# Optimization experiments

Hardware: AMD Instinct MI355X
Metric: run time of the kernel (lower is better)

The kernel has to match this reference:

```python
import jax, jax.numpy as jnp
import numpy as np

N = 100000      # nodes
E = 1600000     # edges (avg degree 16)
D = 128         # feature dim (in_dim == out_dim)
ALPHA = 0.1     # initial-residual mixing
BETA = 0.5      # identity-mapping / linear mixing


def setup_inputs() -> dict:
    key = jax.random.key(0)
    k1, k2, k3, k4, k5 = jax.random.split(key, 5)
    features = jax.random.normal(k1, (N, D), dtype=jnp.float32)
    initial_features = jax.random.normal(k2, (N, D), dtype=jnp.float32)
    # xavier_uniform with relu gain sqrt(2): bound = gain * sqrt(6/(fan_in+fan_out))
    bound = np.sqrt(2.0) * np.sqrt(6.0 / (D + D))
    W = jax.random.uniform(k5, (D, D), dtype=jnp.float32, minval=-bound, maxval=bound)
    src = jax.random.randint(k3, (E,), 0, N, dtype=jnp.int32)
    dst = jax.random.randint(k4, (E,), 0, N, dtype=jnp.int32)
    return {"features": features, "initial_features": initial_features,
            "W": W, "src": src, "dst": dst}


def reference(features, initial_features, W, src, dst):
    # symmetric degree normalization (edge weights are all ones)
    degs = jax.ops.segment_sum(jnp.ones((E,), features.dtype), dst, num_segments=N)
    norm = jnp.power(jnp.maximum(degs, 1.0), -0.5)[:, None]          # [N,1]
    h = features * norm                                               # [N,D]
    # message passing: m_e = h[src_e] * w_e (w=1); aggregate sum into dst
    agg = jax.ops.segment_sum(h[src], dst, num_segments=N)            # [N,D]
    h = agg * norm
    # alpha initial-residual, beta identity-mapped linear combine
    h = (1.0 - ALPHA) * h + ALPHA * initial_features
    h = (1.0 - BETA) * h + BETA * (h @ W.T)
    return jax.nn.relu(h)
```

## Files before the change

### kernel.cpp

```cpp
#include <hip/hip_runtime.h>
#include <math.h>

#define D 128
#define THREADS 256
#define BS 512
#define MAXB 1024
#define BIN_T 512
#define EPT 16
#define BIN_CHUNK (BIN_T * EPT)

typedef __attribute__((ext_vector_type(8))) short s16x8;
typedef __attribute__((ext_vector_type(4))) float f32x4;
typedef __attribute__((ext_vector_type(4))) float f4;
typedef __attribute__((ext_vector_type(4))) unsigned u4;

__device__ __forceinline__ unsigned short f2bf(float f) {
    unsigned u = __float_as_uint(f);
    u += 0x7FFFu + ((u >> 16) & 1u);
    return (unsigned short)(u >> 16);
}
__device__ __forceinline__ float bflo(unsigned u) { return __uint_as_float(u << 16); }
__device__ __forceinline__ float bfhi(unsigned u) { return __uint_as_float(u & 0xFFFF0000u); }


__global__ __launch_bounds__(THREADS) void k_hist(const int* __restrict__ dst,
                                                  int* __restrict__ bcnt,
                                                  int E, int nbuck) {
    __shared__ int lh[MAXB];
    for (int b = threadIdx.x; b < nbuck; b += THREADS) lh[b] = 0;
    __syncthreads();
    const int stride = gridDim.x * THREADS;
    for (int e = blockIdx.x * THREADS + threadIdx.x; e < E; e += stride)
        atomicAdd(&lh[dst[e] >> 9], 1);
    __syncthreads();
    for (int b = threadIdx.x; b < nbuck; b += THREADS) {
        const int v = lh[b];
        if (v) atomicAdd(&bcnt[b], v);
    }
}

__global__ __launch_bounds__(MAXB) void k_scan(const int* __restrict__ bcnt,
                                               int* __restrict__ bbase,
                                               int* __restrict__ bcur, int nbuck) {
    __shared__ int sh[MAXB];
    const int tid = threadIdx.x;
    const int v = (tid < nbuck) ? bcnt[tid] : 0;
    sh[tid] = v;
    __syncthreads();
    for (int s = 1; s < MAXB; s <<= 1) {
        const int t = (tid >= s) ? sh[tid - s] : 0;
        __syncthreads();
        sh[tid] += t;
        __syncthreads();
    }
    if (tid < nbuck) {
        const int ex = sh[tid] - v;
        bbase[tid] = ex;
        bcur[tid] = ex;
    }
    if (tid == nbuck - 1) bbase[nbuck] = sh[tid];
}

__global__ __launch_bounds__(BIN_T) void k_bin(const int* __restrict__ src,
                                               const int* __restrict__ dst,
                                               int* __restrict__ bcur,
                                               unsigned* __restrict__ ebuf,
                                               int E, int nbuck) {
    __shared__ int lh[MAXB];
    __shared__ int lbase[MAXB];
    const int tid = threadIdx.x;
    for (int b = tid; b < nbuck; b += BIN_T) lh[b] = 0;
    __syncthreads();
    const int base = blockIdx.x * BIN_CHUNK;
    int bk[EPT];
    unsigned pk[EPT];
#pragma unroll
    for (int k = 0; k < EPT; ++k) {
        const int e = base + k * BIN_T + tid;
        if (e < E) {
            const int d = dst[e];
            bk[k] = d >> 9;
            pk[k] = ((unsigned)src[e] << 9) | (unsigned)(d & (BS - 1));
            atomicAdd(&lh[bk[k]], 1);
        } else {
            bk[k] = -1;
        }
    }
    __syncthreads();
    for (int b = tid; b < nbuck; b += BIN_T) {
        const int v = lh[b];
        lbase[b] = v ? atomicAdd(&bcur[b], v) : 0;
        lh[b] = 0;
    }
    __syncthreads();
#pragma unroll
    for (int k = 0; k < EPT; ++k) {
        if (bk[k] >= 0) {
            const int pos = lbase[bk[k]] + atomicAdd(&lh[bk[k]], 1);
            ebuf[pos] = pk[k];
        }
    }
}

__global__ __launch_bounds__(BS) void k_csr(const int* __restrict__ bbase,
                                            const unsigned* __restrict__ ebuf,
                                            int* __restrict__ csr,
                                            int* __restrict__ off,
                                            float* __restrict__ normf,
                                            int n, int nbuck) {
    __shared__ int cnt[BS];
    __shared__ int ex[BS];
    const int b = blockIdx.x, tid = threadIdx.x;
    const int lo = bbase[b], hi = bbase[b + 1];
    cnt[tid] = 0;
    __syncthreads();
    for (int e = lo + tid; e < hi; e += BS)
        atomicAdd(&cnt[ebuf[e] & (BS - 1)], 1);
    __syncthreads();
    const int deg = cnt[tid];
    ex[tid] = deg;
    __syncthreads();
    for (int s = 1; s < BS; s <<= 1) {
        const int t = (tid >= s) ? ex[tid - s] : 0;
        __syncthreads();
        ex[tid] += t;
        __syncthreads();
    }
    const int excl = ex[tid] - deg;
    const int node = b * BS + tid;
    if (node < n) {
        off[node] = lo + excl;
        normf[node] = rsqrtf(fmaxf((float)deg, 1.0f));
    }
    if (b == nbuck - 1 && tid == 0) off[n] = bbase[nbuck];
    cnt[tid] = excl;
    __syncthreads();
    for (int e = lo + tid; e < hi; e += BS) {
        const unsigned pe = ebuf[e];
        const int p = atomicAdd(&cnt[pe & (BS - 1)], 1);
        csr[lo + p] = (int)(pe >> 9);
    }
}

__global__ __launch_bounds__(THREADS) void k_scale(
    const float* __restrict__ f, const float* __restrict__ nrm,
    uint4* __restrict__ hb, int n) {
    int c = blockIdx.x * THREADS + threadIdx.x;
    if (c >= n * 16) return;
    float nv = nrm[c >> 4];
    const f4* fp = (const f4*)f;
    const f4 a = __builtin_nontemporal_load(fp + c * 2);
    const f4 b = __builtin_nontemporal_load(fp + c * 2 + 1);
    uint4 o;
    o.x = f2bf(a.x * nv) | ((unsigned)f2bf(a.y * nv) << 16);
    o.y = f2bf(a.z * nv) | ((unsigned)f2bf(a.w * nv) << 16);
    o.z = f2bf(b.x * nv) | ((unsigned)f2bf(b.y * nv) << 16);
    o.w = f2bf(b.z * nv) | ((unsigned)f2bf(b.w * nv) << 16);
    hb[c] = o;
}

__global__ __launch_bounds__(THREADS) void k_gather_csr(
    const uint4* __restrict__ hb, const float* __restrict__ initf,
    const int* __restrict__ off, const int* __restrict__ csr,
    const float* __restrict__ normf, uint4* __restrict__ tb, int n) {
    const int g = (blockIdx.x * THREADS + threadIdx.x) >> 4;
    if (g >= n) return;
    const int gl = threadIdx.x & 15;

    float acc[8] = {0.f, 0.f, 0.f, 0.f, 0.f, 0.f, 0.f, 0.f};

#define ROW(S)                                                      \
    {                                                               \
        const uint4 r = hb[(size_t)(S)*16 + gl];                    \
        acc[0] += bflo(r.x); acc[1] += bfhi(r.x);                   \
        acc[2] += bflo(r.y); acc[3] += bfhi(r.y);                   \
        acc[4] += bflo(r.z); acc[5] += bfhi(r.z);                   \
        acc[6] += bflo(r.w); acc[7] += bfhi(r.w);                   \
    }
    const int begin = off[g], end = off[g + 1];
    int j = begin;
    for (; j + 4 <= end; j += 4) {
        const int s0 = csr[j], s1 = csr[j + 1], s2 = csr[j + 2], s3 = csr[j + 3];
        ROW(s0); ROW(s1); ROW(s2); ROW(s3);
    }
    for (; j < end; ++j) ROW(csr[j]);
#undef ROW

    const float nv = 0.9f * normf[g];
    const f4* iv = (const f4*)(initf + (size_t)g * D);
    const f4 i0 = __builtin_nontemporal_load(iv + gl * 2);
    const f4 i1 = __builtin_nontemporal_load(iv + gl * 2 + 1);
    float t[8];
    t[0] = nv * acc[0] + 0.1f * i0.x; t[1] = nv * acc[1] + 0.1f * i0.y;
    t[2] = nv * acc[2] + 0.1f * i0.z; t[3] = nv * acc[3] + 0.1f * i0.w;
    t[4] = nv * acc[4] + 0.1f * i1.x; t[5] = nv * acc[5] + 0.1f * i1.y;
    t[6] = nv * acc[6] + 0.1f * i1.z; t[7] = nv * acc[7] + 0.1f * i1.w;
    u4 o;
    o.x = f2bf(t[0]) | ((unsigned)f2bf(t[1]) << 16);
    o.y = f2bf(t[2]) | ((unsigned)f2bf(t[3]) << 16);
    o.z = f2bf(t[4]) | ((unsigned)f2bf(t[5]) << 16);
    o.w = f2bf(t[6]) | ((unsigned)f2bf(t[7]) << 16);
    __builtin_nontemporal_store(o, (u4*)tb + (size_t)g * 16 + gl);
}

__device__ __forceinline__ void stage_M(const float* __restrict__ W,
                                        uint4* __restrict__ sMt, int tid) {
    for (int c = tid; c < D * 16; c += THREADS) {
        const int j = c >> 4, kc = c & 15;
        const float* wr = W + j * D + kc * 8;
        float m[8];
#pragma unroll
        for (int q = 0; q < 8; ++q) m[q] = 0.5f * wr[q];
        const int dj = j - kc * 8;
        if (dj >= 0 && dj < 8) m[dj] += 0.5f;
        uint4 o;
        o.x = f2bf(m[0]) | ((unsigned)f2bf(m[1]) << 16);
        o.y = f2bf(m[2]) | ((unsigned)f2bf(m[3]) << 16);
        o.z = f2bf(m[4]) | ((unsigned)f2bf(m[5]) << 16);
        o.w = f2bf(m[6]) | ((unsigned)f2bf(m[7]) << 16);
        sMt[j * 16 + (kc ^ (j & 7))] = o;
    }
}

__device__ __forceinline__ void gemm_tile(const uint4* __restrict__ sMt,
                                          const uint4* __restrict__ sT,
                                          float* __restrict__ out,
                                          int base, int n, int lane, int wave) {
    const int l15 = lane & 15, lq = lane >> 4;
    const int mt = wave & 1, ntb = (wave >> 1) * 4;
    const int nr = mt * 16 + l15;
    s16x8 a[4];
#pragma unroll
    for (int ks = 0; ks < 4; ++ks)
        a[ks] = *reinterpret_cast<const s16x8*>(
            &sT[nr * 16 + ((ks * 4 + lq) ^ (nr & 7))]);

#pragma unroll
    for (int tnt = 0; tnt < 4; ++tnt) {
        const int nt = ntb + tnt;
        const int jr = nt * 16 + l15;
        f32x4 c = {0.f, 0.f, 0.f, 0.f};
#pragma unroll
        for (int ks = 0; ks < 4; ++ks) {
            const s16x8 b = *reinterpret_cast<const s16x8*>(
                &sMt[jr * 16 + ((ks * 4 + lq) ^ (jr & 7))]);
            c = __builtin_amdgcn_mfma_f32_16x16x32_bf16(a[ks], b, c, 0, 0, 0);
        }
        const int col = nt * 16 + l15;
        const int row0 = base + mt * 16 + lq * 4;
#pragma unroll
        for (int r = 0; r < 4; ++r) {
            const int node = row0 + r;
            if (node < n)
                __builtin_nontemporal_store(fmaxf(c[r], 0.f),
                                            &out[(size_t)node * D + col]);
        }
    }
}

__global__ __launch_bounds__(THREADS) void k_gemm_tb(
    const float* __restrict__ W, const uint4* __restrict__ tb,
    float* __restrict__ out, int n, int numTiles) {
    __shared__ uint4 sMt[D * 16];
    __shared__ uint4 sT[32 * 16];
    const int tid = threadIdx.x;
    stage_M(W, sMt, tid);
    __syncthreads();

    const int sn = tid >> 3;
    const int c0 = (tid & 7) * 2;
    const int wave = tid >> 6, lane = tid & 63;

    for (int tile = blockIdx.x; tile < numTiles; tile += gridDim.x) {
        const int base = tile << 5;
        {
            const int node = base + sn;
#pragma unroll
            for (int s = 0; s < 2; ++s) {
                const int cc = c0 + s;
                uint4 o;
                if (node < n) {
                    const u4 t = __builtin_nontemporal_load(
                        (const u4*)tb + (size_t)node * 16 + cc);
                    o.x = t.x; o.y = t.y; o.z = t.z; o.w = t.w;
                } else {
                    o.x = o.y = o.z = o.w = 0u;
                }
                sT[sn * 16 + (cc ^ (sn & 7))] = o;
            }
        }
        __syncthreads();
        gemm_tile(sMt, sT, out, base, n, lane, wave);
        __syncthreads();
    }
}

__global__ __launch_bounds__(THREADS) void k_build1(
    const int* __restrict__ src, const int* __restrict__ dst,
    int* __restrict__ head, int2* __restrict__ p, int E) {
    int e = blockIdx.x * THREADS + threadIdx.x;
    if (e < E) {
        int nx = atomicExch(&head[dst[e]], e);
        p[e] = make_int2(nx, src[e]);
    }
}

__global__ __launch_bounds__(THREADS) void k_normwalk1(
    const int* __restrict__ head, const int2* __restrict__ p,
    float* __restrict__ normf, int n) {
    int i = blockIdx.x * THREADS + threadIdx.x;
    if (i >= n) return;
    int c = head[i], cnt = 0;
    while (c >= 0) { ++cnt; c = p[c].x; }
    normf[i] = rsqrtf(fmaxf((float)cnt, 1.0f));
}

__global__ __launch_bounds__(THREADS) void k_gatherchain(
    const float* __restrict__ features, const float* __restrict__ initf,
    const int* __restrict__ head, const int2* __restrict__ p,
    const float* __restrict__ normf, float* __restrict__ out, int n) {
    const int g = (blockIdx.x * THREADS + threadIdx.x) >> 4;
    if (g >= n) return;
    const int gl = threadIdx.x & 15;
    float acc[8] = {0.f, 0.f, 0.f, 0.f, 0.f, 0.f, 0.f, 0.f};
    int c = head[g];
    while (c >= 0) {
        const int2 pc = p[c];
        const float w = normf[pc.y];
        const float4* fr = (const float4*)(features + (size_t)pc.y * D);
        const float4 f0 = fr[gl * 2], f1 = fr[gl * 2 + 1];
        acc[0] += f0.x * w; acc[1] += f0.y * w;
        acc[2] += f0.z * w; acc[3] += f0.w * w;
        acc[4] += f1.x * w; acc[5] += f1.y * w;
        acc[6] += f1.z * w; acc[7] += f1.w * w;
        c = pc.x;
    }
    const float nv = 0.9f * normf[g];
    const float4* iv = (const float4*)(initf + (size_t)g * D);
    const float4 i0 = iv[gl * 2], i1 = iv[gl * 2 + 1];
    float4 t0, t1;
    t0.x = nv * acc[0] + 0.1f * i0.x; t0.y = nv * acc[1] + 0.1f * i0.y;
    t0.z = nv * acc[2] + 0.1f * i0.z; t0.w = nv * acc[3] + 0.1f * i0.w;
    t1.x = nv * acc[4] + 0.1f * i1.x; t1.y = nv * acc[5] + 0.1f * i1.y;
    t1.z = nv * acc[6] + 0.1f * i1.z; t1.w = nv * acc[7] + 0.1f * i1.w;
    float4* orow = (float4*)(out + (size_t)g * D);
    orow[gl * 2] = t0;
    orow[gl * 2 + 1] = t1;
}

__global__ __launch_bounds__(THREADS) void k_gemm_ip(
    const float* __restrict__ W, float* __restrict__ out, int n, int numTiles) {
    __shared__ uint4 sMt[D * 16];
    __shared__ uint4 sT[32 * 16];
    const int tid = threadIdx.x;
    stage_M(W, sMt, tid);
    __syncthreads();
    const int sn = tid >> 3;
    const int c0 = (tid & 7) * 2;
    const int wave = tid >> 6, lane = tid & 63;
    for (int tile = blockIdx.x; tile < numTiles; tile += gridDim.x) {
        const int base = tile << 5;
        {
            const int node = base + sn;
#pragma unroll
            for (int s = 0; s < 2; ++s) {
                const int cc = c0 + s;
                uint4 o;
                if (node < n) {
                    const float4* tr = (const float4*)(out + (size_t)node * D);
                    const float4 a = tr[cc * 2], b = tr[cc * 2 + 1];
                    o.x = f2bf(a.x) | ((unsigned)f2bf(a.y) << 16);
                    o.y = f2bf(a.z) | ((unsigned)f2bf(a.w) << 16);
                    o.z = f2bf(b.x) | ((unsigned)f2bf(b.y) << 16);
                    o.w = f2bf(b.z) | ((unsigned)f2bf(b.w) << 16);
                } else {
                    o.x = o.y = o.z = o.w = 0u;
                }
                sT[sn * 16 + (cc ^ (sn & 7))] = o;
            }
        }
        __syncthreads();
        gemm_tile(sMt, sT, out, base, n, lane, wave);
        __syncthreads();
    }
}

extern "C" void kernel_launch(void* const* d_in, const int* in_sizes, int n_in,
                              void* d_out, int out_size, void* d_ws, size_t ws_size,
                              hipStream_t stream) {
    const float* features = (const float*)d_in[0];
    const float* initf    = (const float*)d_in[1];
    const float* W        = (const float*)d_in[2];
    const int*   src      = (const int*)d_in[3];
    const int*   dst      = (const int*)d_in[4];
    float* out = (float*)d_out;

    const int n = in_sizes[0] / D;
    const int E = in_sizes[3];
    if (n <= 0) return;

    const int nbuck = (n + BS - 1) / BS;
    const int numTiles = (n + 31) >> 5;
    const int gridT = numTiles < 1024 ? numTiles : 1024;
    const int gridG = (int)(((size_t)n * 16 + THREADS - 1) / THREADS);

    const size_t nA   = ((size_t)n * 4 + 15) & ~(size_t)15;
    const size_t oA   = ((size_t)(n + 1) * 4 + 15) & ~(size_t)15;
    const size_t bA   = ((size_t)(MAXB + 1) * 4 + 15) & ~(size_t)15;
    const size_t eA   = ((size_t)E * 4 + 15) & ~(size_t)15;
    const size_t cA   = ((size_t)E * 4 + 15) & ~(size_t)15;
    const size_t hbA  = (size_t)n * 256;
    const size_t tbA  = (size_t)n * 256;
    const size_t needMain = nA + oA + 3 * bA + eA + cA + hbA + tbA;

    if (nbuck <= MAXB && n <= (1 << 23) && ws_size >= needMain) {
        char* w = (char*)d_ws;
        float*    normf = (float*)w;              w += nA;
        int*      off   = (int*)w;                w += oA;
        int*      bcnt  = (int*)w;                w += bA;
        int*      bbase = (int*)w;                w += bA;
        int*      bcur  = (int*)w;                w += bA;
        unsigned* ebuf  = (unsigned*)w;           w += eA;
        int*      csr   = (int*)w;                w += cA;
        uint4*    hb    = (uint4*)w;              w += hbA;
        uint4*    tb    = (uint4*)w;

        hipMemsetAsync(bcnt, 0, (size_t)(MAXB + 1) * 4, stream);
        k_hist<<<256, THREADS, 0, stream>>>(dst, bcnt, E, nbuck);
        k_scan<<<1, MAXB, 0, stream>>>(bcnt, bbase, bcur, nbuck);
        k_bin<<<(E + BIN_CHUNK - 1) / BIN_CHUNK, BIN_T, 0, stream>>>(
            src, dst, bcur, ebuf, E, nbuck);
        k_csr<<<nbuck, BS, 0, stream>>>(bbase, ebuf, csr, off, normf, n, nbuck);
        k_scale<<<(n * 16 + THREADS - 1) / THREADS, THREADS, 0, stream>>>(
            features, normf, hb, n);
        k_gather_csr<<<gridG, THREADS, 0, stream>>>(hb, initf, off, csr, normf, tb, n);
        k_gemm_tb<<<gridT, THREADS, 0, stream>>>(W, tb, out, n, numTiles);
    } else {
        const size_t pA = ((size_t)E * 8 + 15) & ~(size_t)15;
        float* normf = (float*)d_ws;
        int*   head  = (int*)((char*)d_ws + nA);
        int2*  p     = (int2*)((char*)d_ws + 2 * nA);
        if (ws_size < 2 * nA + pA) return;
        hipMemsetAsync(head, 0xFF, (size_t)n * 4, stream);
        k_build1<<<(E + THREADS - 1) / THREADS, THREADS, 0, stream>>>(src, dst, head, p, E);
        k_normwalk1<<<(n + THREADS - 1) / THREADS, THREADS, 0, stream>>>(head, p, normf, n);
        k_gatherchain<<<gridG, THREADS, 0, stream>>>(features, initf, head, p, normf, out, n);
        k_gemm_ip<<<gridT, THREADS, 0, stream>>>(W, out, n, numTiles);
    }
}
```

Before: 186.2 us.

## Fuse feature scaling into CSR build, partition edges by source quarter, widen gather

The CSR build now sorts each node's neighbor list into four source-index ranges and stores the per-range counts, so the gather visits source rows in phases that roughly match the source-row partition and should improve L2 locality of the bf16 feature reads. The separate scale kernel is folded into the CSR kernel, which removes one launch. The gather now gives each node 64 threads (four sub-groups striding over its edges) and combines them with cross-lane shuffles, trading fewer nodes per block for more memory parallelism per node. The histogram kernel also reads dst as int4 vectors. The costs are a larger shared-memory count array in the CSR kernel and per-range counts capped at 16 bits.

Measured after the change: 194.6 us. +4.5%, slower.

```diff
diff --git a/kernel.cpp b/kernel.cpp
--- a/kernel.cpp
+++ b/kernel.cpp
@@ -22,7 +22,6 @@
 __device__ __forceinline__ float bflo(unsigned u) { return __uint_as_float(u << 16); }
 __device__ __forceinline__ float bfhi(unsigned u) { return __uint_as_float(u & 0xFFFF0000u); }
 
-
 __global__ __launch_bounds__(THREADS) void k_hist(const int* __restrict__ dst,
                                                   int* __restrict__ bcnt,
                                                   int E, int nbuck) {
@@ -30,8 +29,17 @@
     for (int b = threadIdx.x; b < nbuck; b += THREADS) lh[b] = 0;
     __syncthreads();
     const int stride = gridDim.x * THREADS;
-    for (int e = blockIdx.x * THREADS + threadIdx.x; e < E; e += stride)
-        atomicAdd(&lh[dst[e] >> 9], 1);
+    const int E4 = E >> 2;
+    const int4* dst4 = (const int4*)dst;
+    for (int i = blockIdx.x * THREADS + threadIdx.x; i < E4; i += stride) {
+        const int4 d = dst4[i];
+        atomicAdd(&lh[d.x >> 9], 1);
+        atomicAdd(&lh[d.y >> 9], 1);
+        atomicAdd(&lh[d.z >> 9], 1);
+        atomicAdd(&lh[d.w >> 9], 1);
+    }
+    if (blockIdx.x == 0 && threadIdx.x < (E & 3))
+        atomicAdd(&lh[dst[(E & ~3) + threadIdx.x] >> 9], 1);
     __syncthreads();
     for (int b = threadIdx.x; b < nbuck; b += THREADS) {
         const int v = lh[b];
@@ -104,20 +112,30 @@
 
 __global__ __launch_bounds__(BS) void k_csr(const int* __restrict__ bbase,
                                             const unsigned* __restrict__ ebuf,
+                                            const float* __restrict__ features,
                                             int* __restrict__ csr,
                                             int* __restrict__ off,
+                                            uint2* __restrict__ pcnt,
                                             float* __restrict__ normf,
-                                            int n, int nbuck) {
-    __shared__ int cnt[BS];
+                                            uint4* __restrict__ hb,
+                                            int n, int nbuck, unsigned cut) {
+    __shared__ int cnt[BS * 4];
     __shared__ int ex[BS];
     const int b = blockIdx.x, tid = threadIdx.x;
     const int lo = bbase[b], hi = bbase[b + 1];
-    cnt[tid] = 0;
-    __syncthreads();
-    for (int e = lo + tid; e < hi; e += BS)
-        atomicAdd(&cnt[ebuf[e] & (BS - 1)], 1);
-    __syncthreads();
-    const int deg = cnt[tid];
+#pragma unroll
+    for (int q = 0; q < 4; ++q) cnt[tid * 4 + q] = 0;
+    __syncthreads();
+    for (int e = lo + tid; e < hi; e += BS) {
+        const unsigned pe = ebuf[e];
+        const unsigned s = pe >> 9;
+        const int q = (s >= cut) + (s >= 2 * cut) + (s >= 3 * cut);
+        atomicAdd(&cnt[(int)(pe & (BS - 1)) * 4 + q], 1);
+    }
+    __syncthreads();
+    int c0 = cnt[tid * 4], c1 = cnt[tid * 4 + 1],
+        c2 = cnt[tid * 4 + 2], c3 = cnt[tid * 4 + 3];
+    const int deg = c0 + c1 + c2 + c3;
     ex[tid] = deg;
     __syncthreads();
     for (int s = 1; s < BS; s <<= 1) {
@@ -128,79 +146,97 @@
     }
     const int excl = ex[tid] - deg;
     const int node = b * BS + tid;
+    const float nrm = rsqrtf(fmaxf((float)deg, 1.0f));
     if (node < n) {
         off[node] = lo + excl;
-        normf[node] = rsqrtf(fmaxf((float)deg, 1.0f));
+        pcnt[node] = make_uint2((unsigned)c0 | ((unsigned)c1 << 16),
+                                (unsigned)c2 | ((unsigned)c3 << 16));
+        normf[node] = nrm;
     }
     if (b == nbuck - 1 && tid == 0) off[n] = bbase[nbuck];
-    cnt[tid] = excl;
-    __syncthreads();
+    int run = excl;
+    cnt[tid * 4 + 0] = run; run += c0;
+    cnt[tid * 4 + 1] = run; run += c1;
+    cnt[tid * 4 + 2] = run; run += c2;
+    cnt[tid * 4 + 3] = run;
+    __syncthreads();
+    ex[tid] = __float_as_int(nrm);
     for (int e = lo + tid; e < hi; e += BS) {
         const unsigned pe = ebuf[e];
-        const int p = atomicAdd(&cnt[pe & (BS - 1)], 1);
-        csr[lo + p] = (int)(pe >> 9);
-    }
-}
-
-__global__ __launch_bounds__(THREADS) void k_scale(
-    const float* __restrict__ f, const float* __restrict__ nrm,
-    uint4* __restrict__ hb, int n) {
-    int c = blockIdx.x * THREADS + threadIdx.x;
-    if (c >= n * 16) return;
-    float nv = nrm[c >> 4];
-    const f4* fp = (const f4*)f;
-    const f4 a = __builtin_nontemporal_load(fp + c * 2);
-    const f4 b = __builtin_nontemporal_load(fp + c * 2 + 1);
-    uint4 o;
-    o.x = f2bf(a.x * nv) | ((unsigned)f2bf(a.y * nv) << 16);
-    o.y = f2bf(a.z * nv) | ((unsigned)f2bf(a.w * nv) << 16);
-    o.z = f2bf(b.x * nv) | ((unsigned)f2bf(b.y * nv) << 16);
-    o.w = f2bf(b.z * nv) | ((unsigned)f2bf(b.w * nv) << 16);
-    hb[c] = o;
+        const unsigned s = pe >> 9;
+        const int q = (s >= cut) + (s >= 2 * cut) + (s >= 3 * cut);
+        const int p = atomicAdd(&cnt[(int)(pe & (BS - 1)) * 4 + q], 1);
+        csr[lo + p] = (int)s;
+    }
+    __syncthreads();
+    const f4* fp = (const f4*)features;
+    for (int idx = tid; idx < BS * 16; idx += BS) {
+        const int nl = idx >> 4;
+        const int gnode = b * BS + nl;
+        if (gnode >= n) break;
+        const float nv = __int_as_float(ex[nl]);
+        const size_t C = (size_t)gnode * 16 + (idx & 15);
+        const f4 a = __builtin_nontemporal_load(fp + C * 2);
+        const f4 bb = __builtin_nontemporal_load(fp + C * 2 + 1);
+        uint4 o;
+        o.x = f2bf(a.x * nv) | ((unsigned)f2bf(a.y * nv) << 16);
+        o.y = f2bf(a.z * nv) | ((unsigned)f2bf(a.w * nv) << 16);
+        o.z = f2bf(bb.x * nv) | ((unsigned)f2bf(bb.y * nv) << 16);
+        o.w = f2bf(bb.z * nv) | ((unsigned)f2bf(bb.w * nv) << 16);
+        hb[C] = o;
+    }
 }
 
 __global__ __launch_bounds__(THREADS) void k_gather_csr(
     const uint4* __restrict__ hb, const float* __restrict__ initf,
-    const int* __restrict__ off, const int* __restrict__ csr,
-    const float* __restrict__ normf, uint4* __restrict__ tb, int n) {
-    const int g = (blockIdx.x * THREADS + threadIdx.x) >> 4;
+    const int* __restrict__ off, const uint2* __restrict__ pcnt,
+    const int* __restrict__ csr, const float* __restrict__ normf,
+    uint4* __restrict__ tb, int n) {
+    const int g = blockIdx.x * 4 + (threadIdx.x >> 6);
     if (g >= n) return;
+    const int sub = (threadIdx.x >> 4) & 3;
     const int gl = threadIdx.x & 15;
 
     float acc[8] = {0.f, 0.f, 0.f, 0.f, 0.f, 0.f, 0.f, 0.f};
-
-#define ROW(S)                                                      \
-    {                                                               \
-        const uint4 r = hb[(size_t)(S)*16 + gl];                    \
-        acc[0] += bflo(r.x); acc[1] += bfhi(r.x);                   \
-        acc[2] += bflo(r.y); acc[3] += bfhi(r.y);                   \
-        acc[4] += bflo(r.z); acc[5] += bfhi(r.z);                   \
-        acc[6] += bflo(r.w); acc[7] += bfhi(r.w);                   \
-    }
-    const int begin = off[g], end = off[g + 1];
-    int j = begin;
-    for (; j + 4 <= end; j += 4) {
-        const int s0 = csr[j], s1 = csr[j + 1], s2 = csr[j + 2], s3 = csr[j + 3];
-        ROW(s0); ROW(s1); ROW(s2); ROW(s3);
-    }
-    for (; j < end; ++j) ROW(csr[j]);
-#undef ROW
-
-    const float nv = 0.9f * normf[g];
-    const f4* iv = (const f4*)(initf + (size_t)g * D);
-    const f4 i0 = __builtin_nontemporal_load(iv + gl * 2);
-    const f4 i1 = __builtin_nontemporal_load(iv + gl * 2 + 1);
-    float t[8];
-    t[0] = nv * acc[0] + 0.1f * i0.x; t[1] = nv * acc[1] + 0.1f * i0.y;
-    t[2] = nv * acc[2] + 0.1f * i0.z; t[3] = nv * acc[3] + 0.1f * i0.w;
-    t[4] = nv * acc[4] + 0.1f * i1.x; t[5] = nv * acc[5] + 0.1f * i1.y;
-    t[6] = nv * acc[6] + 0.1f * i1.z; t[7] = nv * acc[7] + 0.1f * i1.w;
-    u4 o;
-    o.x = f2bf(t[0]) | ((unsigned)f2bf(t[1]) << 16);
-    o.y = f2bf(t[2]) | ((unsigned)f2bf(t[3]) << 16);
-    o.z = f2bf(t[4]) | ((unsigned)f2bf(t[5]) << 16);
-    o.w = f2bf(t[6]) | ((unsigned)f2bf(t[7]) << 16);
-    __builtin_nontemporal_store(o, (u4*)tb + (size_t)g * 16 + gl);
+    int j = off[g];
+    const uint2 pc = pcnt[g];
+    const int lens[4] = {(int)(pc.x & 0xFFFFu), (int)(pc.x >> 16),
+                         (int)(pc.y & 0xFFFFu), (int)(pc.y >> 16)};
+#pragma unroll 1
+    for (int p = 0; p < 4; ++p) {
+        const int end = j + lens[p];
+        for (int jj = j + sub; jj < end; jj += 4) {
+            const int s = csr[jj];
+            const uint4 r = hb[(size_t)s * 16 + gl];
+            acc[0] += bflo(r.x); acc[1] += bfhi(r.x);
+            acc[2] += bflo(r.y); acc[3] += bfhi(r.y);
+            acc[4] += bflo(r.z); acc[5] += bfhi(r.z);
+            acc[6] += bflo(r.w); acc[7] += bfhi(r.w);
+        }
+        j = end;
+    }
+#pragma unroll
+    for (int q = 0; q < 8; ++q) {
+        acc[q] += __shfl_xor(acc[q], 16);
+        acc[q] += __shfl_xor(acc[q], 32);
+    }
+    if (sub == 0) {
+        const float nv = 0.9f * normf[g];
+        const f4* iv = (const f4*)(initf + (size_t)g * D);
+        const f4 i0 = __builtin_nontemporal_load(iv + gl * 2);
+        const f4 i1 = __builtin_nontemporal_load(iv + gl * 2 + 1);
+        float t[8];
+        t[0] = nv * acc[0] + 0.1f * i0.x; t[1] = nv * acc[1] + 0.1f * i0.y;
+        t[2] = nv * acc[2] + 0.1f * i0.z; t[3] = nv * acc[3] + 0.1f * i0.w;
+        t[4] = nv * acc[4] + 0.1f * i1.x; t[5] = nv * acc[5] + 0.1f * i1.y;
+        t[6] = nv * acc[6] + 0.1f * i1.z; t[7] = nv * acc[7] + 0.1f * i1.w;
+        u4 o;
+        o.x = f2bf(t[0]) | ((unsigned)f2bf(t[1]) << 16);
+        o.y = f2bf(t[2]) | ((unsigned)f2bf(t[3]) << 16);
+        o.z = f2bf(t[4]) | ((unsigned)f2bf(t[5]) << 16);
+        o.w = f2bf(t[6]) | ((unsigned)f2bf(t[7]) << 16);
+        __builtin_nontemporal_store(o, (u4*)tb + (size_t)g * 16 + gl);
+    }
 }
 
 __device__ __forceinline__ void stage_M(const float* __restrict__ W,
@@ -402,21 +438,22 @@
     const int nbuck = (n + BS - 1) / BS;
     const int numTiles = (n + 31) >> 5;
     const int gridT = numTiles < 1024 ? numTiles : 1024;
-    const int gridG = (int)(((size_t)n * 16 + THREADS - 1) / THREADS);
 
     const size_t nA   = ((size_t)n * 4 + 15) & ~(size_t)15;
     const size_t oA   = ((size_t)(n + 1) * 4 + 15) & ~(size_t)15;
+    const size_t pcA  = ((size_t)n * 8 + 15) & ~(size_t)15;
     const size_t bA   = ((size_t)(MAXB + 1) * 4 + 15) & ~(size_t)15;
     const size_t eA   = ((size_t)E * 4 + 15) & ~(size_t)15;
     const size_t cA   = ((size_t)E * 4 + 15) & ~(size_t)15;
     const size_t hbA  = (size_t)n * 256;
     const size_t tbA  = (size_t)n * 256;
-    const size_t needMain = nA + oA + 3 * bA + eA + cA + hbA + tbA;
+    const size_t needMain = nA + oA + pcA + 3 * bA + eA + cA + hbA + tbA;
 
     if (nbuck <= MAXB && n <= (1 << 23) && ws_size >= needMain) {
         char* w = (char*)d_ws;
         float*    normf = (float*)w;              w += nA;
         int*      off   = (int*)w;                w += oA;
+        uint2*    pcnt  = (uint2*)w;              w += pcA;
         int*      bcnt  = (int*)w;                w += bA;
         int*      bbase = (int*)w;                w += bA;
         int*      bcur  = (int*)w;                w += bA;
@@ -425,15 +462,17 @@
         uint4*    hb    = (uint4*)w;              w += hbA;
         uint4*    tb    = (uint4*)w;
 
+        const unsigned cut = ((unsigned)n + 3) >> 2;
+
         hipMemsetAsync(bcnt, 0, (size_t)(MAXB + 1) * 4, stream);
         k_hist<<<256, THREADS, 0, stream>>>(dst, bcnt, E, nbuck);
         k_scan<<<1, MAXB, 0, stream>>>(bcnt, bbase, bcur, nbuck);
         k_bin<<<(E + BIN_CHUNK - 1) / BIN_CHUNK, BIN_T, 0, stream>>>(
             src, dst, bcur, ebuf, E, nbuck);
-        k_csr<<<nbuck, BS, 0, stream>>>(bbase, ebuf, csr, off, normf, n, nbuck);
-        k_scale<<<(n * 16 + THREADS - 1) / THREADS, THREADS, 0, stream>>>(
-            features, normf, hb, n);
-        k_gather_csr<<<gridG, THREADS, 0, stream>>>(hb, initf, off, csr, normf, tb, n);
+        k_csr<<<nbuck, BS, 0, stream>>>(bbase, ebuf, features, csr, off, pcnt,
+                                        normf, hb, n, nbuck, cut);
+        k_gather_csr<<<(n + 3) / 4, THREADS, 0, stream>>>(
+            hb, initf, off, pcnt, csr, normf, tb, n);
         k_gemm_tb<<<gridT, THREADS, 0, stream>>>(W, tb, out, n, numTiles);
     } else {
         const size_t pA = ((size_t)E * 8 + 15) & ~(size_t)15;
@@ -441,6 +480,7 @@
         int*   head  = (int*)((char*)d_ws + nA);
         int2*  p     = (int2*)((char*)d_ws + 2 * nA);
         if (ws_size < 2 * nA + pA) return;
+        const int gridG = (int)(((size_t)n * 16 + THREADS - 1) / THREADS);
         hipMemsetAsync(head, 0xFF, (size_t)n * 4, stream);
         k_build1<<<(E + THREADS - 1) / THREADS, THREADS, 0, stream>>>(src, dst, head, p, E);
         k_normwalk1<<<(n + THREADS - 1) / THREADS, THREADS, 0, stream>>>(head, p, normf, n);
```

## Replace histogram+scan with fixed-capacity bucket slabs and fuse scaling into CSR build

Applied to the files above, without the earlier changes.

Drops the separate histogram, scan and memset passes by giving each 512-node bucket a fixed slab of CAP slots. Edges that do not fit go to an overflow list stored in the tb buffer. The feature scaling to bf16 moves into the CSR-build kernel, and offsets are stored as an (offset, degree) pair. This removes one full pass over dst and several launches, at the cost of scanning the overflow list in every CSR block and of a larger workspace.

New measurement: 168.6 us. 1.1x faster.

```diff
diff --git a/kernel.cpp b/kernel.cpp
--- a/kernel.cpp
+++ b/kernel.cpp
@@ -5,6 +5,7 @@
 #define THREADS 256
 #define BS 512
 #define MAXB 1024
+#define CAP 9216
 #define BIN_T 512
 #define EPT 16
 #define BIN_CHUNK (BIN_T * EPT)
@@ -22,49 +23,19 @@
 __device__ __forceinline__ float bflo(unsigned u) { return __uint_as_float(u << 16); }
 __device__ __forceinline__ float bfhi(unsigned u) { return __uint_as_float(u & 0xFFFF0000u); }
 
-
-__global__ __launch_bounds__(THREADS) void k_hist(const int* __restrict__ dst,
-                                                  int* __restrict__ bcnt,
-                                                  int E, int nbuck) {
-    __shared__ int lh[MAXB];
-    for (int b = threadIdx.x; b < nbuck; b += THREADS) lh[b] = 0;
-    __syncthreads();
-    const int stride = gridDim.x * THREADS;
-    for (int e = blockIdx.x * THREADS + threadIdx.x; e < E; e += stride)
-        atomicAdd(&lh[dst[e] >> 9], 1);
-    __syncthreads();
-    for (int b = threadIdx.x; b < nbuck; b += THREADS) {
-        const int v = lh[b];
-        if (v) atomicAdd(&bcnt[b], v);
-    }
-}
-
-__global__ __launch_bounds__(MAXB) void k_scan(const int* __restrict__ bcnt,
-                                               int* __restrict__ bbase,
-                                               int* __restrict__ bcur, int nbuck) {
-    __shared__ int sh[MAXB];
-    const int tid = threadIdx.x;
-    const int v = (tid < nbuck) ? bcnt[tid] : 0;
-    sh[tid] = v;
-    __syncthreads();
-    for (int s = 1; s < MAXB; s <<= 1) {
-        const int t = (tid >= s) ? sh[tid - s] : 0;
-        __syncthreads();
-        sh[tid] += t;
-        __syncthreads();
-    }
-    if (tid < nbuck) {
-        const int ex = sh[tid] - v;
-        bbase[tid] = ex;
-        bcur[tid] = ex;
-    }
-    if (tid == nbuck - 1) bbase[nbuck] = sh[tid];
+__global__ __launch_bounds__(THREADS) void k_init(int* __restrict__ bcur,
+                                                  int* __restrict__ ocnt, int nbuck) {
+    const int b = blockIdx.x * THREADS + threadIdx.x;
+    if (b < nbuck) bcur[b] = b * CAP;
+    if (b == 0) *ocnt = 0;
 }
 
 __global__ __launch_bounds__(BIN_T) void k_bin(const int* __restrict__ src,
                                                const int* __restrict__ dst,
                                                int* __restrict__ bcur,
                                                unsigned* __restrict__ ebuf,
+                                               int2* __restrict__ ovf,
+                                               int* __restrict__ ocnt,
                                                int E, int nbuck) {
     __shared__ int lh[MAXB];
     __shared__ int lbase[MAXB];
@@ -97,25 +68,40 @@
     for (int k = 0; k < EPT; ++k) {
         if (bk[k] >= 0) {
             const int pos = lbase[bk[k]] + atomicAdd(&lh[bk[k]], 1);
-            ebuf[pos] = pk[k];
-        }
-    }
-}
-
-__global__ __launch_bounds__(BS) void k_csr(const int* __restrict__ bbase,
-                                            const unsigned* __restrict__ ebuf,
+            if (pos < (bk[k] + 1) * CAP) {
+                ebuf[pos] = pk[k];
+            } else {
+                const int op = atomicAdd(ocnt, 1);
+                ovf[op] = make_int2((int)pk[k], bk[k]);
+            }
+        }
+    }
+}
+
+__global__ __launch_bounds__(BS) void k_csr(const unsigned* __restrict__ ebuf,
+                                            const int* __restrict__ bcur,
+                                            const int2* __restrict__ ovf,
+                                            const int* __restrict__ ocnt,
+                                            const float* __restrict__ features,
                                             int* __restrict__ csr,
-                                            int* __restrict__ off,
+                                            int2* __restrict__ offdeg,
                                             float* __restrict__ normf,
+                                            uint4* __restrict__ hb,
                                             int n, int nbuck) {
     __shared__ int cnt[BS];
     __shared__ int ex[BS];
     const int b = blockIdx.x, tid = threadIdx.x;
-    const int lo = bbase[b], hi = bbase[b + 1];
+    const int lo = b * CAP;
+    const int hi = min(bcur[b], lo + CAP);
+    const int oc = *ocnt;
     cnt[tid] = 0;
     __syncthreads();
     for (int e = lo + tid; e < hi; e += BS)
         atomicAdd(&cnt[ebuf[e] & (BS - 1)], 1);
+    for (int i = tid; i < oc; i += BS) {
+        const int2 o = ovf[i];
+        if (o.y == b) atomicAdd(&cnt[(unsigned)o.x & (BS - 1)], 1);
+    }
     __syncthreads();
     const int deg = cnt[tid];
     ex[tid] = deg;
@@ -128,40 +114,50 @@
     }
     const int excl = ex[tid] - deg;
     const int node = b * BS + tid;
+    const float nrm = rsqrtf(fmaxf((float)deg, 1.0f));
     if (node < n) {
-        off[node] = lo + excl;
-        normf[node] = rsqrtf(fmaxf((float)deg, 1.0f));
-    }
-    if (b == nbuck - 1 && tid == 0) off[n] = bbase[nbuck];
+        offdeg[node] = make_int2(lo + excl, deg);
+        normf[node] = nrm;
+    }
     cnt[tid] = excl;
     __syncthreads();
+    ex[tid] = __float_as_int(nrm);
+    const int csrEnd = nbuck * CAP;
     for (int e = lo + tid; e < hi; e += BS) {
         const unsigned pe = ebuf[e];
         const int p = atomicAdd(&cnt[pe & (BS - 1)], 1);
-        csr[lo + p] = (int)(pe >> 9);
-    }
-}
-
-__global__ __launch_bounds__(THREADS) void k_scale(
-    const float* __restrict__ f, const float* __restrict__ nrm,
-    uint4* __restrict__ hb, int n) {
-    int c = blockIdx.x * THREADS + threadIdx.x;
-    if (c >= n * 16) return;
-    float nv = nrm[c >> 4];
-    const f4* fp = (const f4*)f;
-    const f4 a = __builtin_nontemporal_load(fp + c * 2);
-    const f4 b = __builtin_nontemporal_load(fp + c * 2 + 1);
-    uint4 o;
-    o.x = f2bf(a.x * nv) | ((unsigned)f2bf(a.y * nv) << 16);
-    o.y = f2bf(a.z * nv) | ((unsigned)f2bf(a.w * nv) << 16);
-    o.z = f2bf(b.x * nv) | ((unsigned)f2bf(b.y * nv) << 16);
-    o.w = f2bf(b.z * nv) | ((unsigned)f2bf(b.w * nv) << 16);
-    hb[c] = o;
+        if (lo + p < csrEnd) csr[lo + p] = (int)(pe >> 9);
+    }
+    for (int i = tid; i < oc; i += BS) {
+        const int2 o = ovf[i];
+        if (o.y == b) {
+            const unsigned pe = (unsigned)o.x;
+            const int p = atomicAdd(&cnt[pe & (BS - 1)], 1);
+            if (lo + p < csrEnd) csr[lo + p] = (int)(pe >> 9);
+        }
+    }
+    __syncthreads();
+    const f4* fp = (const f4*)features;
+    for (int idx = tid; idx < BS * 16; idx += BS) {
+        const int nl = idx >> 4;
+        const int gnode = b * BS + nl;
+        if (gnode >= n) break;
+        const float nv = __int_as_float(ex[nl]);
+        const size_t C = (size_t)gnode * 16 + (idx & 15);
+        const f4 a = __builtin_nontemporal_load(fp + C * 2);
+        const f4 bb = __builtin_nontemporal_load(fp + C * 2 + 1);
+        uint4 o;
+        o.x = f2bf(a.x * nv) | ((unsigned)f2bf(a.y * nv) << 16);
+        o.y = f2bf(a.z * nv) | ((unsigned)f2bf(a.w * nv) << 16);
+        o.z = f2bf(bb.x * nv) | ((unsigned)f2bf(bb.y * nv) << 16);
+        o.w = f2bf(bb.z * nv) | ((unsigned)f2bf(bb.w * nv) << 16);
+        hb[C] = o;
+    }
 }
 
 __global__ __launch_bounds__(THREADS) void k_gather_csr(
     const uint4* __restrict__ hb, const float* __restrict__ initf,
-    const int* __restrict__ off, const int* __restrict__ csr,
+    const int2* __restrict__ offdeg, const int* __restrict__ csr,
     const float* __restrict__ normf, uint4* __restrict__ tb, int n) {
     const int g = (blockIdx.x * THREADS + threadIdx.x) >> 4;
     if (g >= n) return;
@@ -177,7 +173,8 @@
         acc[4] += bflo(r.z); acc[5] += bfhi(r.z);                   \
         acc[6] += bflo(r.w); acc[7] += bfhi(r.w);                   \
     }
-    const int begin = off[g], end = off[g + 1];
+    const int2 od = offdeg[g];
+    const int begin = od.x, end = od.x + od.y;
     int j = begin;
     for (; j + 4 <= end; j += 4) {
         const int s0 = csr[j], s1 = csr[j + 1], s2 = csr[j + 2], s3 = csr[j + 3];
@@ -404,36 +401,32 @@
     const int gridT = numTiles < 1024 ? numTiles : 1024;
     const int gridG = (int)(((size_t)n * 16 + THREADS - 1) / THREADS);
 
+    const size_t odA  = ((size_t)n * 8 + 15) & ~(size_t)15;
     const size_t nA   = ((size_t)n * 4 + 15) & ~(size_t)15;
-    const size_t oA   = ((size_t)(n + 1) * 4 + 15) & ~(size_t)15;
-    const size_t bA   = ((size_t)(MAXB + 1) * 4 + 15) & ~(size_t)15;
-    const size_t eA   = ((size_t)E * 4 + 15) & ~(size_t)15;
-    const size_t cA   = ((size_t)E * 4 + 15) & ~(size_t)15;
+    const size_t bA   = ((size_t)MAXB * 4 + 16);
+    const size_t slabA = ((size_t)nbuck * CAP * 4 + 15) & ~(size_t)15;
     const size_t hbA  = (size_t)n * 256;
     const size_t tbA  = (size_t)n * 256;
-    const size_t needMain = nA + oA + 3 * bA + eA + cA + hbA + tbA;
+    const size_t needMain = odA + nA + bA + 2 * slabA + hbA + tbA;
 
     if (nbuck <= MAXB && n <= (1 << 23) && ws_size >= needMain) {
         char* w = (char*)d_ws;
-        float*    normf = (float*)w;              w += nA;
-        int*      off   = (int*)w;                w += oA;
-        int*      bcnt  = (int*)w;                w += bA;
-        int*      bbase = (int*)w;                w += bA;
-        int*      bcur  = (int*)w;                w += bA;
-        unsigned* ebuf  = (unsigned*)w;           w += eA;
-        int*      csr   = (int*)w;                w += cA;
-        uint4*    hb    = (uint4*)w;              w += hbA;
-        uint4*    tb    = (uint4*)w;
-
-        hipMemsetAsync(bcnt, 0, (size_t)(MAXB + 1) * 4, stream);
-        k_hist<<<256, THREADS, 0, stream>>>(dst, bcnt, E, nbuck);
-        k_scan<<<1, MAXB, 0, stream>>>(bcnt, bbase, bcur, nbuck);
+        int2*     offdeg = (int2*)w;              w += odA;
+        float*    normf  = (float*)w;             w += nA;
+        int*      bcur   = (int*)w;
+        int*      ocnt   = (int*)(w + (size_t)MAXB * 4);  w += bA;
+        unsigned* ebuf   = (unsigned*)w;          w += slabA;
+        int*      csr    = (int*)w;               w += slabA;
+        uint4*    hb     = (uint4*)w;             w += hbA;
+        uint4*    tb     = (uint4*)w;
+        int2*     ovf    = (int2*)tb;
+
+        k_init<<<(nbuck + THREADS - 1) / THREADS, THREADS, 0, stream>>>(bcur, ocnt, nbuck);
         k_bin<<<(E + BIN_CHUNK - 1) / BIN_CHUNK, BIN_T, 0, stream>>>(
-            src, dst, bcur, ebuf, E, nbuck);
-        k_csr<<<nbuck, BS, 0, stream>>>(bbase, ebuf, csr, off, normf, n, nbuck);
-        k_scale<<<(n * 16 + THREADS - 1) / THREADS, THREADS, 0, stream>>>(
-            features, normf, hb, n);
-        k_gather_csr<<<gridG, THREADS, 0, stream>>>(hb, initf, off, csr, normf, tb, n);
+            src, dst, bcur, ebuf, ovf, ocnt, E, nbuck);
+        k_csr<<<nbuck, BS, 0, stream>>>(ebuf, bcur, ovf, ocnt, features,
+                                        csr, offdeg, normf, hb, n, nbuck);
+        k_gather_csr<<<gridG, THREADS, 0, stream>>>(hb, initf, offdeg, csr, normf, tb, n);
         k_gemm_tb<<<gridT, THREADS, 0, stream>>>(W, tb, out, n, numTiles);
     } else {
         const size_t pA = ((size_t)E * 8 + 15) & ~(size_t)15;
```
